# Optimization experiments

Measured on AMD Instinct MI355X. Metric: run time of the kernel, lower is better.

## Reference

```python
import jax, jax.numpy as jnp
import numpy as np

B, S, D, H = 2, 2048, 1024, 16
HD = D // H

def setup_inputs() -> dict:
    key = jax.random.key(0)
    k1, k2, k3 = jax.random.split(key, 3)
    x = jax.random.normal(k1, (B, S, D), dtype=jnp.float32)
    c_attn_w = jax.random.normal(k2, (D, 3 * D), dtype=jnp.float32) * 0.02
    c_attn_b = jnp.zeros((3 * D,), dtype=jnp.float32)
    c_proj_w = jax.random.normal(k3, (D, D), dtype=jnp.float32) * 0.02
    c_proj_b = jnp.zeros((D,), dtype=jnp.float32)
    return {"x": x, "c_attn_w": c_attn_w, "c_attn_b": c_attn_b,
            "c_proj_w": c_proj_w, "c_proj_b": c_proj_b}

def reference(x, c_attn_w, c_attn_b, c_proj_w, c_proj_b):
    bsz, seq_len, d = x.shape
    # Conv1D: addmm(bias, x, weight) -> x @ W + b
    qkv = x @ c_attn_w + c_attn_b                      # [B,S,3D]
    xq, xk, xv = jnp.split(qkv, 3, axis=-1)
    # [B,H,S,hd]
    xq = xq.reshape(bsz, seq_len, H, HD).transpose(0, 2, 1, 3)
    xk = xk.reshape(bsz, seq_len, H, HD).transpose(0, 2, 1, 3)
    xv = xv.reshape(bsz, seq_len, H, HD).transpose(0, 2, 1, 3)
    # Eager attention: QK^T / sqrt(hd), causal mask, softmax, AV
    scale = jnp.asarray(HD, x.dtype) ** 0.5
    attn_weights = jnp.einsum('bhqd,bhkd->bhqk', xq, xk) / scale
    causal = jnp.tril(jnp.ones((seq_len, seq_len), dtype=bool))
    mask_value = jnp.finfo(attn_weights.dtype).min
    attn_weights = jnp.where(causal[None, None], attn_weights, mask_value)
    attn_weights = jax.nn.softmax(attn_weights, axis=-1)
    attn_output = jnp.einsum('bhqk,bhkd->bhqd', attn_weights, xv)  # [B,H,S,hd]
    attn_output = attn_output.transpose(0, 2, 1, 3).reshape(bsz, seq_len, d)
    attn_output = attn_output @ c_proj_w + c_proj_b
    return attn_output
```

## Files before the change

### kernel.cpp

```cpp
#include <hip/hip_runtime.h>
#include <hip/hip_bf16.h>
#include <stdint.h>

#define S_LEN 2048
#define D_DIM 1024
#define N_HEAD 16

typedef unsigned short u16;
typedef __attribute__((ext_vector_type(4))) float f32x4;
typedef __attribute__((ext_vector_type(16))) float f32x16;
typedef __attribute__((ext_vector_type(8))) short bf16x8;
typedef __attribute__((ext_vector_type(4))) unsigned short u16x4;
typedef __attribute__((ext_vector_type(4))) float flt4;

#define MFMA16(a, b, c) __builtin_amdgcn_mfma_f32_16x16x32_bf16((a), (b), (c), 0, 0, 0)
#define MFMA32(a, b, c) __builtin_amdgcn_mfma_f32_32x32x16_bf16((a), (b), (c), 0, 0, 0)

__device__ __forceinline__ u16 f32_bf16(float f) {
    union { float f; uint32_t u; } x;
    x.f = f;
    uint32_t r = (x.u + 0x7FFFu + ((x.u >> 16) & 1u)) >> 16;
    return (u16)r;
}

__device__ __forceinline__ uint32_t pack2(float a, float b) {
    __hip_bfloat162 h = __float22bfloat162_rn(float2{a, b});
    return *(uint32_t*)&h;
}

__device__ __forceinline__ void gload_lds16(const void* g, void* l) {
    __builtin_amdgcn_global_load_lds(
        (const __attribute__((address_space(1))) unsigned int*)(uintptr_t)g,
        (__attribute__((address_space(3))) unsigned int*)(uint32_t)(uintptr_t)l,
        16, 0, 0);
}


__global__ __launch_bounds__(256) void cvt_bf16_kernel(const float* __restrict__ in,
                                                       u16* __restrict__ out, int n) {
    int i = (blockIdx.x * 256 + threadIdx.x) * 4;
    if (i < n) {
        flt4 v = *(const flt4*)(in + i);
        u16x4 u;
        u[0] = f32_bf16(v[0]); u[1] = f32_bf16(v[1]);
        u[2] = f32_bf16(v[2]); u[3] = f32_bf16(v[3]);
        *(u16x4*)(out + i) = u;
    }
}

__global__ __launch_bounds__(256) void transpose_cvt_kernel(const float* __restrict__ in,
                                                            u16* __restrict__ out,
                                                            int R, int C) {
    __shared__ float tile[32][33];
    int tc = blockIdx.x * 32, tr = blockIdx.y * 32;
    int lx = threadIdx.x & 31, ly = threadIdx.x >> 5;
#pragma unroll
    for (int i = 0; i < 32; i += 8)
        tile[ly + i][lx] = in[(size_t)(tr + ly + i) * C + tc + lx];
    __syncthreads();
#pragma unroll
    for (int i = 0; i < 32; i += 8)
        out[(size_t)(tc + ly + i) * R + tr + lx] = f32_bf16(tile[lx][ly + i]);
}


template <int MODE>
__global__ __launch_bounds__(256)
void gemm_bt_kernel(const u16* __restrict__ A, const u16* __restrict__ Bt,
                    const float* __restrict__ bias,
                    float* __restrict__ outF,
                    u16* __restrict__ qo, u16* __restrict__ ko, u16* __restrict__ vto,
                    int M, int N, int K) {
    __shared__ u16 As[128 * 32];
    __shared__ u16 Bs[128 * 32];
    const int tid = threadIdx.x;
    const int w = tid >> 6, lane = tid & 63;
    const int lr = lane & 15, lg = lane >> 4;
    const int bm = blockIdx.y * 128, bn = blockIdx.x * 128;
    const int wr = w >> 1, wc = w & 1;

    f32x4 acc[4][4];
#pragma unroll
    for (int m = 0; m < 4; m++)
#pragma unroll
        for (int n = 0; n < 4; n++) acc[m][n] = (f32x4){0.f, 0.f, 0.f, 0.f};

    const u16* Abase = A + (size_t)(bm + (tid >> 2)) * K + (tid & 3) * 8;
    const u16* Bbase = Bt + (size_t)(bn + (tid >> 2)) * K + (tid & 3) * 8;
    u16* AsW = As + w * 512;
    u16* BsW = Bs + w * 512;

    for (int kt = 0; kt < K; kt += 32) {
        gload_lds16(Abase + kt, AsW);
        gload_lds16(Abase + kt + (size_t)64 * K, AsW + 2048);
        gload_lds16(Bbase + kt, BsW);
        gload_lds16(Bbase + kt + (size_t)64 * K, BsW + 2048);
        __syncthreads();

        bf16x8 a[4], b[4];
        const bf16x8* Av = (const bf16x8*)As;
        const bf16x8* Bv = (const bf16x8*)Bs;
#pragma unroll
        for (int m = 0; m < 4; m++) a[m] = Av[(wr * 64 + m * 16 + lr) * 4 + lg];
#pragma unroll
        for (int n = 0; n < 4; n++) b[n] = Bv[(wc * 64 + n * 16 + lr) * 4 + lg];
#pragma unroll
        for (int m = 0; m < 4; m++)
#pragma unroll
            for (int n = 0; n < 4; n++)
                acc[m][n] = MFMA16(a[m], b[n], acc[m][n]);
        __syncthreads();
    }

    const int rowb = bm + wr * 64, colb = bn + wc * 64;
    if (MODE == 0) {
#pragma unroll
        for (int m = 0; m < 4; m++)
#pragma unroll
            for (int j = 0; j < 4; j++) {
                int r = rowb + m * 16 + lg * 4 + j;
                size_t base = (size_t)r * N;
#pragma unroll
                for (int n = 0; n < 4; n++) {
                    int c = colb + n * 16 + lr;
                    outF[base + c] = acc[m][n][j] + bias[c];
                }
            }
    } else {
#pragma unroll
        for (int m = 0; m < 4; m++)
#pragma unroll
            for (int j = 0; j < 4; j++) {
                int r = rowb + m * 16 + lg * 4 + j;
                int bb = r >> 11, s = r & (S_LEN - 1);
#pragma unroll
                for (int n = 0; n < 4; n++) {
                    int c = colb + n * 16 + lr;
                    float v = acc[m][n][j] + bias[c];
                    int part = c >> 10, cc = c & (D_DIM - 1);
                    if (part == 0) v *= 0.125f;
                    u16 bv = f32_bf16(v);
                    int h = cc >> 6, d = cc & 63;
                    size_t bh = (size_t)(bb * N_HEAD + h);
                    if (part == 0)      qo[(bh * S_LEN + s) * 64 + d] = bv;
                    else if (part == 1) ko[(bh * S_LEN + s) * 64 + d] = bv;
                    else                vto[(bh * 64 + d) * S_LEN + s] = bv;
                }
            }
    }
}


#define PSTRIDE 40

__global__ __launch_bounds__(256)
void flash_attn_kernel(const u16* __restrict__ Qg, const u16* __restrict__ Kg,
                       const u16* __restrict__ Vt, u16* __restrict__ Og) {
    const int id = blockIdx.x;
    const int xcd = id & 7, slot = id >> 3;
    const int bh = xcd * 4 + (slot & 3);
    const int p  = slot >> 2;
    const int w = threadIdx.x >> 6, lane = threadIdx.x & 63;
    const int qt = (w == 0) ? p : (w == 1) ? 31 - p : (w == 2) ? 32 + p : 63 - p;
    const int qbase = qt * 32;
    const int ql = lane & 31, hi = lane >> 5;
    const int swz = (ql & 3) << 3;

    const u16* Qh = Qg + (size_t)bh * S_LEN * 64;
    const u16* Kh = Kg + (size_t)bh * S_LEN * 64;
    const u16* Vh = Vt + (size_t)bh * 64 * S_LEN;

    __shared__ __align__(16) u16 plds[4][32 * PSTRIDE];
    u16* pw = plds[w];

    bf16x8 qf[4];
#pragma unroll
    for (int c = 0; c < 4; c++)
        qf[c] = *(const bf16x8*)(Qh + (size_t)(qbase + ql) * 64 + c * 16 + hi * 8);

    f32x16 ot0 = {}, ot1 = {};
    float m = -1e30f, l = 0.f;

    bf16x8 kn[4], vn[4];
#pragma unroll
    for (int c = 0; c < 4; c++)
        kn[c] = *(const bf16x8*)(Kh + (size_t)ql * 64 + c * 16 + hi * 8);
#pragma unroll
    for (int u = 0; u < 4; u++)
        vn[u] = *(const bf16x8*)(Vh + (size_t)((u >> 1) * 32 + ql) * S_LEN + (u & 1) * 16 + hi * 8);

    for (int t = 0; t <= qt; ++t) {
        bf16x8 ka[4] = {kn[0], kn[1], kn[2], kn[3]};
        bf16x8 va[4] = {vn[0], vn[1], vn[2], vn[3]};
        if (t < qt) {
            const size_t kvn = (size_t)(t + 1) * 32;
#pragma unroll
            for (int c = 0; c < 4; c++)
                kn[c] = *(const bf16x8*)(Kh + (kvn + ql) * 64 + c * 16 + hi * 8);
#pragma unroll
            for (int u = 0; u < 4; u++)
                vn[u] = *(const bf16x8*)(Vh + (size_t)((u >> 1) * 32 + ql) * S_LEN + kvn + (u & 1) * 16 + hi * 8);
        }

        f32x16 st = {};
#pragma unroll
        for (int c = 0; c < 4; c++) st = MFMA32(ka[c], qf[c], st);

        float s[16];
#pragma unroll
        for (int r = 0; r < 16; r++) s[r] = st[r];
        if (t == qt) {
#pragma unroll
            for (int r = 0; r < 16; r++) {
                int kvl = ((r & 3) + 8 * (r >> 2)) + 4 * hi;
                if (kvl > ql) s[r] = -1e30f;
            }
        }

        float t0 = fmaxf(s[0], s[1]),   t1 = fmaxf(s[2], s[3]);
        float t2 = fmaxf(s[4], s[5]),   t3 = fmaxf(s[6], s[7]);
        float t4 = fmaxf(s[8], s[9]),   t5 = fmaxf(s[10], s[11]);
        float t6 = fmaxf(s[12], s[13]), t7 = fmaxf(s[14], s[15]);
        t0 = fmaxf(t0, t1); t2 = fmaxf(t2, t3); t4 = fmaxf(t4, t5); t6 = fmaxf(t6, t7);
        float tmax = fmaxf(fmaxf(t0, t2), fmaxf(t4, t6));
        tmax = fmaxf(tmax, __shfl_xor(tmax, 32));

        float corr = 1.f;
        if (!__all(tmax <= m)) {
            float mnew = fmaxf(m, tmax);
            corr = __expf(m - mnew);
            m = mnew;
            ot0 *= corr;
            ot1 *= corr;
        }

        float pe[16];
        float rs = 0.f;
#pragma unroll
        for (int r = 0; r < 16; r++) { pe[r] = __expf(s[r] - m); rs += pe[r]; }
        rs += __shfl_xor(rs, 32);
        l = l * corr + rs;

#pragma unroll
        for (int rp = 0; rp < 8; rp++) {
            const int r = rp * 2;
            const int kv = ((r & 3) + 8 * (r >> 2)) + 4 * hi;
            *(uint32_t*)(pw + ql * PSTRIDE + (kv ^ swz)) = pack2(pe[r], pe[r + 1]);
        }
        bf16x8 pa0 = *(const bf16x8*)(pw + ql * PSTRIDE + ((hi * 8) ^ swz));
        bf16x8 pa1 = *(const bf16x8*)(pw + ql * PSTRIDE + ((16 + hi * 8) ^ swz));

        ot0 = MFMA32(va[0], pa0, ot0);
        ot0 = MFMA32(va[1], pa1, ot0);
        ot1 = MFMA32(va[2], pa0, ot1);
        ot1 = MFMA32(va[3], pa1, ot1);
    }

    const float inv = 1.f / l;
    const int b = bh >> 4, hh = bh & 15;
    u16* orow = Og + ((size_t)(b * S_LEN) + qbase + ql) * D_DIM + hh * 64;
#pragma unroll
    for (int rp = 0; rp < 8; rp++) {
        const int r = rp * 2;
        const int d = ((r & 3) + 8 * (r >> 2)) + 4 * hi;
        *(uint32_t*)(orow + d) = pack2(ot0[r] * inv, ot0[r + 1] * inv);
        *(uint32_t*)(orow + 32 + d) = pack2(ot1[r] * inv, ot1[r + 1] * inv);
    }
}


extern "C" void kernel_launch(void* const* d_in, const int* in_sizes, int n_in,
                              void* d_out, int out_size, void* d_ws, size_t ws_size,
                              hipStream_t stream) {
    const float* x  = (const float*)d_in[0];
    const float* w1 = (const float*)d_in[1];
    const float* b1 = (const float*)d_in[2];
    const float* w2 = (const float*)d_in[3];
    const float* b2 = (const float*)d_in[4];
    float* out = (float*)d_out;

    u16* ws  = (u16*)d_ws;
    u16* xb  = ws;
    u16* w1t = xb  + 4096 * 1024;
    u16* w2t = w1t + 3072 * 1024;
    u16* q   = w2t + 1024 * 1024;
    u16* k   = q   + 4194304;
    u16* vt  = k   + 4194304;
    u16* x2  = vt  + 4194304;

    cvt_bf16_kernel<<<dim3(4096), dim3(256), 0, stream>>>(x, xb, 4096 * 1024);
    transpose_cvt_kernel<<<dim3(3072 / 32, 1024 / 32), dim3(256), 0, stream>>>(w1, w1t, 1024, 3072);
    transpose_cvt_kernel<<<dim3(1024 / 32, 1024 / 32), dim3(256), 0, stream>>>(w2, w2t, 1024, 1024);

    gemm_bt_kernel<1><<<dim3(3072 / 128, 4096 / 128), dim3(256), 0, stream>>>(
        xb, w1t, b1, nullptr, q, k, vt, 4096, 3072, 1024);

    flash_attn_kernel<<<dim3(512), dim3(256), 0, stream>>>(q, k, vt, x2);

    gemm_bt_kernel<0><<<dim3(1024 / 128, 4096 / 128), dim3(256), 0, stream>>>(
        x2, w2t, b2, out, nullptr, nullptr, nullptr, 4096, 1024, 1024);
}
```

Measured before the change: 235.2 us.

## Use permlane32 swap for P transpose, exp2 softmax, single-wave attention blocks

```diff
diff --git a/kernel.cpp b/kernel.cpp
--- a/kernel.cpp
+++ b/kernel.cpp
@@ -138,7 +138,7 @@
                     int c = colb + n * 16 + lr;
                     float v = acc[m][n][j] + bias[c];
                     int part = c >> 10, cc = c & (D_DIM - 1);
-                    if (part == 0) v *= 0.125f;
+                    if (part == 0) v *= 0.125f * 1.44269504f;
                     u16 bv = f32_bf16(v);
                     int h = cc >> 6, d = cc & 63;
                     size_t bh = (size_t)(bb * N_HEAD + h);
@@ -151,27 +151,19 @@
 }
 
 
-#define PSTRIDE 40
-
-__global__ __launch_bounds__(256)
+__global__ __launch_bounds__(64)
 void flash_attn_kernel(const u16* __restrict__ Qg, const u16* __restrict__ Kg,
                        const u16* __restrict__ Vt, u16* __restrict__ Og) {
     const int id = blockIdx.x;
-    const int xcd = id & 7, slot = id >> 3;
-    const int bh = xcd * 4 + (slot & 3);
-    const int p  = slot >> 2;
-    const int w = threadIdx.x >> 6, lane = threadIdx.x & 63;
-    const int qt = (w == 0) ? p : (w == 1) ? 31 - p : (w == 2) ? 32 + p : 63 - p;
+    const int bh = id & 31;
+    const int qt = 63 - (id >> 5);
     const int qbase = qt * 32;
+    const int lane = threadIdx.x;
     const int ql = lane & 31, hi = lane >> 5;
-    const int swz = (ql & 3) << 3;
 
     const u16* Qh = Qg + (size_t)bh * S_LEN * 64;
     const u16* Kh = Kg + (size_t)bh * S_LEN * 64;
     const u16* Vh = Vt + (size_t)bh * 64 * S_LEN;
-
-    __shared__ __align__(16) u16 plds[4][32 * PSTRIDE];
-    u16* pw = plds[w];
 
     bf16x8 qf[4];
 #pragma unroll
@@ -203,8 +195,10 @@
         }
 
         f32x16 st = {};
+        __builtin_amdgcn_s_setprio(1);
 #pragma unroll
         for (int c = 0; c < 4; c++) st = MFMA32(ka[c], qf[c], st);
+        __builtin_amdgcn_s_setprio(0);
 
         float s[16];
 #pragma unroll
@@ -228,7 +222,7 @@
         float corr = 1.f;
         if (!__all(tmax <= m)) {
             float mnew = fmaxf(m, tmax);
-            corr = __expf(m - mnew);
+            corr = __builtin_amdgcn_exp2f(m - mnew);
             m = mnew;
             ot0 *= corr;
             ot1 *= corr;
@@ -237,23 +231,27 @@
         float pe[16];
         float rs = 0.f;
 #pragma unroll
-        for (int r = 0; r < 16; r++) { pe[r] = __expf(s[r] - m); rs += pe[r]; }
+        for (int r = 0; r < 16; r++) { pe[r] = __builtin_amdgcn_exp2f(s[r] - m); rs += pe[r]; }
         rs += __shfl_xor(rs, 32);
         l = l * corr + rs;
 
-#pragma unroll
-        for (int rp = 0; rp < 8; rp++) {
-            const int r = rp * 2;
-            const int kv = ((r & 3) + 8 * (r >> 2)) + 4 * hi;
-            *(uint32_t*)(pw + ql * PSTRIDE + (kv ^ swz)) = pack2(pe[r], pe[r + 1]);
-        }
-        bf16x8 pa0 = *(const bf16x8*)(pw + ql * PSTRIDE + ((hi * 8) ^ swz));
-        bf16x8 pa1 = *(const bf16x8*)(pw + ql * PSTRIDE + ((16 + hi * 8) ^ swz));
-
-        ot0 = MFMA32(va[0], pa0, ot0);
-        ot0 = MFMA32(va[1], pa1, ot0);
-        ot1 = MFMA32(va[2], pa0, ot1);
-        ot1 = MFMA32(va[3], pa1, ot1);
+        uint32_t wv[8];
+#pragma unroll
+        for (int sp = 0; sp < 8; sp++) wv[sp] = pack2(pe[2 * sp], pe[2 * sp + 1]);
+        auto r02 = __builtin_amdgcn_permlane32_swap(wv[0], wv[2], false, false);
+        auto r13 = __builtin_amdgcn_permlane32_swap(wv[1], wv[3], false, false);
+        auto r46 = __builtin_amdgcn_permlane32_swap(wv[4], wv[6], false, false);
+        auto r57 = __builtin_amdgcn_permlane32_swap(wv[5], wv[7], false, false);
+        union { uint32_t u[4]; bf16x8 v; } pa0, pa1;
+        pa0.u[0] = r02[0]; pa0.u[1] = r13[0]; pa0.u[2] = r02[1]; pa0.u[3] = r13[1];
+        pa1.u[0] = r46[0]; pa1.u[1] = r57[0]; pa1.u[2] = r46[1]; pa1.u[3] = r57[1];
+
+        __builtin_amdgcn_s_setprio(1);
+        ot0 = MFMA32(va[0], pa0.v, ot0);
+        ot0 = MFMA32(va[1], pa1.v, ot0);
+        ot1 = MFMA32(va[2], pa0.v, ot1);
+        ot1 = MFMA32(va[3], pa1.v, ot1);
+        __builtin_amdgcn_s_setprio(0);
     }
 
     const float inv = 1.f / l;
@@ -295,7 +293,7 @@
     gemm_bt_kernel<1><<<dim3(3072 / 128, 4096 / 128), dim3(256), 0, stream>>>(
         xb, w1t, b1, nullptr, q, k, vt, 4096, 3072, 1024);
 
-    flash_attn_kernel<<<dim3(512), dim3(256), 0, stream>>>(q, k, vt, x2);
+    flash_attn_kernel<<<dim3(2048), dim3(64), 0, stream>>>(q, k, vt, x2);
 
     gemm_bt_kernel<0><<<dim3(1024 / 128, 4096 / 128), dim3(256), 0, stream>>>(
         x2, w2t, b2, out, nullptr, nullptr, nullptr, 4096, 1024, 1024);
```

After: 235.1 us. About the same (-0.0%).
